# Performance work log

Measured on AMD Instinct MI355X. Metric: run time of the kernel, lower is better.

## Reference

```python
import jax, jax.numpy as jnp
import numpy as np
from jax import lax

N, L, C_IN, NOISE_C, COMP, NC = 256, 512, 514, 112, 16, 2
MAIN_IN = NOISE_C + COMP  # 128
FEAT = NC * 4 * L         # 4096

def _conv1d(x, w, b, pad):
    # x [N,C,L], w [O,I,K]
    y = lax.conv_general_dilated(x, w, (1,), [(pad, pad)], dimension_numbers=('NCH', 'OIH', 'NCH'))
    return y + b[None, :, None]

def _bn(x, g, b):
    # BatchNorm1d, training mode: biased batch stats over (N, L)
    m = x.mean(axis=(0, 2), keepdims=True)
    v = x.var(axis=(0, 2), keepdims=True)
    return (x - m) * lax.rsqrt(v + 1e-5) * g[None, :, None] + b[None, :, None]

def _lrelu(x):
    return jnp.where(x >= 0, x, 0.2 * x)

def _pos_encode(length, dim):
    j = np.arange(dim)
    div = 1.0 / np.power(10000.0, 2 * (j[:, None] // 2) / dim)   # [dim,1]
    ang = np.arange(length)[None, :] * div                       # [dim,length]
    ang = np.where((j % 2 == 0)[:, None], np.sin(ang), np.cos(ang))
    return jnp.asarray(ang[None], jnp.float32)                   # [1,dim,length]

def _assemble(circle_prob, slider_prob):
    # Vectorized run-length label expansion equivalent to the per-sample python while-loop.
    # circle_prob [N, L/2, 2], slider_prob [N, L/4, 2] -> [N, L, 3]
    n, B = slider_prob.shape[0], slider_prob.shape[1]
    c = jnp.argmax(circle_prob, -1)
    s = jnp.argmax(slider_prob, -1)
    zc = jnp.zeros(circle_prob.shape[:-1] + (1,), circle_prob.dtype)
    zs = jnp.zeros(slider_prob.shape[:-1] + (1,), slider_prob.dtype)
    cp3 = jnp.concatenate([circle_prob, zc], -1)                                   # insert 0 at class 2
    sp3 = jnp.concatenate([slider_prob[..., :1], zs, slider_prob[..., 1:]], -1)    # insert 0 at class 1
    pad100 = jnp.array([1., 0., 0.], cp3.dtype)
    pad001 = jnp.array([0., 0., 1.], cp3.dtype)
    bidx = jnp.arange(B)[None, :]
    # slider-body blocks: slider run continues and not cut by sequence end
    body = (s == 1) & (bidx < B - 1)
    prev_body = jnp.concatenate([jnp.zeros((n, 1), bool), body[:, :-1]], 1)
    # tail block ends a slider run (either run stops, or boundary block)
    tail = ((s == 1) & (bidx == B - 1)) | ((s == 0) & prev_body)
    # circle emission for each half-step: prob row if predicted circle else pad
    cr0 = jnp.where((c == 1)[..., None], cp3, pad100).reshape(n, B, 2, 3)
    bodyE = body[..., None]
    row0 = jnp.where((body | tail)[..., None], sp3, cr0[:, :, 0, :])
    row1 = jnp.where(bodyE, pad001, pad100)
    row2 = jnp.where(bodyE, pad001, cr0[:, :, 1, :])
    row3 = jnp.where(bodyE, pad001, pad100)
    return jnp.stack([row0, row1, row2, row3], 2).reshape(n, 4 * B, 3)

def _forward(noise, cond_data, gumbel_u, ext_w1, ext_b1, ext_w2, ext_b2, ext_bn_g, ext_bn_b,
             m_w1, m_b1, m_w2, m_b2, m_bn_g, m_bn_b, lin_w, lin_b, circ_w, circ_b, slid_w, slid_b):
    # FeatureExtractor
    x = cond_data.transpose(0, 2, 1)                      # [N, 514, L]
    x = _lrelu(_conv1d(x, ext_w1, ext_b1, 0))             # [N, 32, L]
    cond = _bn(_conv1d(x, ext_w2, ext_b2, 1), ext_bn_g, ext_bn_b)  # [N, 16, L]
    gen_in = jnp.concatenate([cond, noise.transpose(0, 2, 1)], 1) + _pos_encode(L, MAIN_IN)  # [N,128,L]
    h = _lrelu(_conv1d(gen_in, m_w1, m_b1, 3))            # [N, 32, L]
    h = _lrelu(_bn(_conv1d(h, m_w2, m_b2, 1), m_bn_g, m_bn_b))     # [N, 8, L]
    flat = _lrelu(h.reshape(h.shape[0], -1) @ lin_w + lin_b)       # [N, 4096]
    circle_prob = (flat @ circ_w + circ_b).reshape(-1, L // 2, NC)
    slider_prob = (flat @ slid_w + slid_b).reshape(-1, L // 4, NC)
    out = _assemble(circle_prob, slider_prob)             # [N, L, 3]
    # gumbel_softmax(hard=True, tau=1)
    g = -jnp.log(-jnp.log(gumbel_u + 1e-10) + 1e-10)
    logits = out + g
    y_soft = jax.nn.softmax(logits, -1)
    y_hard = jax.nn.one_hot(jnp.argmax(logits, -1), 3, dtype=y_soft.dtype)
    gen_out = y_hard + y_soft - lax.stop_gradient(y_soft)
    return gen_out, cond

def setup_inputs() -> dict:
    key = jax.random.key(0)
    ks = jax.random.split(key, 12)
    def rn(k, shape, fan_in):
        return jax.random.normal(k, shape, jnp.float32) * (1.0 / fan_in) ** 0.5
    return {
        'noise': jax.random.normal(ks[0], (N, L, NOISE_C), jnp.float32),
        'cond_data': jax.random.normal(ks[1], (N, L, C_IN), jnp.float32),
        'gumbel_u': jax.random.uniform(ks[2], (N, L, 3), jnp.float32),
        'ext_w1': rn(ks[3], (C_IN // 16, C_IN, 1), C_IN), 'ext_b1': jnp.zeros(C_IN // 16),
        'ext_w2': rn(ks[4], (COMP, C_IN // 16, 3), 3 * (C_IN // 16)), 'ext_b2': jnp.zeros(COMP),
        'ext_bn_g': jnp.ones(COMP), 'ext_bn_b': jnp.zeros(COMP),
        'm_w1': rn(ks[5], (NC * 16, MAIN_IN, 7), 7 * MAIN_IN), 'm_b1': jnp.zeros(NC * 16),
        'm_w2': rn(ks[6], (NC * 4, NC * 16, 3), 3 * NC * 16), 'm_b2': jnp.zeros(NC * 4),
        'm_bn_g': jnp.ones(NC * 4), 'm_bn_b': jnp.zeros(NC * 4),
        'lin_w': rn(ks[7], (FEAT, FEAT), FEAT), 'lin_b': jnp.zeros(FEAT),
        'circ_w': rn(ks[8], (FEAT, NC * L // 2), FEAT), 'circ_b': jnp.zeros(NC * L // 2),
        'slid_w': rn(ks[9], (FEAT, NC * L // 4), FEAT), 'slid_b': jnp.zeros(NC * L // 4),
    }

def reference(noise, cond_data, gumbel_u, ext_w1, ext_b1, ext_w2, ext_b2, ext_bn_g, ext_bn_b,
              m_w1, m_b1, m_w2, m_b2, m_bn_g, m_bn_b, lin_w, lin_b, circ_w, circ_b, slid_w, slid_b):
    return _forward(noise, cond_data, gumbel_u, ext_w1, ext_b1, ext_w2, ext_b2, ext_bn_g, ext_bn_b,
                    m_w1, m_b1, m_w2, m_b2, m_bn_g, m_bn_b, lin_w, lin_b, circ_w, circ_b, slid_w, slid_b)
```

## Files before the change

kernel.cpp:

```cpp
#include <hip/hip_runtime.h>
#include <math.h>

#define NB 256
#define LL 512
#define CIN 514

__device__ __forceinline__ float lrelu(float x) { return x >= 0.f ? x : 0.2f * x; }

__global__ __launch_bounds__(256) void k_pos(float* __restrict__ pos) {
    int idx = blockIdx.x * 256 + threadIdx.x;
    int c = idx >> 9, l = idx & 511;
    double e = (double)(2 * (c >> 1)) / 128.0;
    double dv = 1.0 / pow(10000.0, e);
    double a = (double)l * dv;
    pos[idx] = (float)((c & 1) ? cos(a) : sin(a));
}

__global__ __launch_bounds__(256) void k_posconv(const float* __restrict__ POS, const float* __restrict__ W,
                                                 const float* __restrict__ bias, float* __restrict__ PC) {
    const int t = threadIdx.x;
    const int o = blockIdx.x >> 4, l0 = (blockIdx.x & 15) * 32;
    const int l = l0 + (t & 31), cs = t >> 5;
    float acc = 0.f;
    for (int ci = 0; ci < 16; ++ci) {
        int c = cs * 16 + ci;
        float wv[7];
#pragma unroll
        for (int k = 0; k < 7; ++k) wv[k] = W[o * 896 + c * 7 + k];
#pragma unroll
        for (int k = 0; k < 7; ++k) {
            int gl = l + k - 3;
            if (gl >= 0 && gl < LL) acc += wv[k] * POS[c * LL + gl];
        }
    }
    __shared__ float red[8][33];
    red[cs][t & 31] = acc;
    __syncthreads();
    if (cs == 0) {
        float s = bias[o];
#pragma unroll
        for (int j = 0; j < 8; ++j) s += red[j][t & 31];
        PC[o * LL + l0 + (t & 31)] = s;
    }
}

__global__ __launch_bounds__(256) void k_conv1(const float* __restrict__ X, const float* __restrict__ W,
                                               float* __restrict__ P0, float* __restrict__ P1) {
    __shared__ __align__(16) float As[16][524];
    __shared__ __align__(16) float Bs[16][36];
    const int t = threadIdx.x;
    const int n = blockIdx.x >> 1, z = blockIdx.x & 1;
    const int kbase = z * 256;
    const int nch = z ? 17 : 16;
    const int tl = t & 63, to = t >> 6;
    const size_t rowbase = (size_t)n * 512 * CIN;

    float acc[8][8];
#pragma unroll
    for (int oi = 0; oi < 8; ++oi)
#pragma unroll
        for (int p = 0; p < 8; ++p) acc[oi][p] = 0.f;

    float2 pf[16];
    float2 pfb;

    {
        const int kb = kbase;
#pragma unroll
        for (int ps = 0; ps < 16; ++ps) {
            int idx = ps * 256 + t;
            int pos = idx >> 3, kp = idx & 7;
            int gk = kb + kp * 2;
            float2 v = {0.f, 0.f};
            if (gk + 1 < CIN) v = *(const float2*)(X + rowbase + (size_t)pos * CIN + gk);
            else if (gk < CIN) v.x = X[rowbase + (size_t)pos * CIN + gk];
            pf[ps] = v;
        }
        {
            int o = t >> 3, kp = t & 7;
            int gk = kb + kp * 2;
            float2 v = {0.f, 0.f};
            if (gk + 1 < CIN) v = *(const float2*)(W + (size_t)o * CIN + gk);
            else if (gk < CIN) v.x = W[(size_t)o * CIN + gk];
            pfb = v;
        }
#pragma unroll
        for (int ps = 0; ps < 16; ++ps) {
            int idx = ps * 256 + t;
            int pos = idx >> 3, kp = idx & 7;
            As[kp * 2][pos] = pf[ps].x;
            As[kp * 2 + 1][pos] = pf[ps].y;
        }
        {
            int o = t >> 3, kp = t & 7;
            Bs[kp * 2][o] = pfb.x;
            Bs[kp * 2 + 1][o] = pfb.y;
        }
    }
    __syncthreads();

    for (int c = 0; c < nch; ++c) {
        if (c + 1 < nch) {
            const int kb = kbase + (c + 1) * 16;
#pragma unroll
            for (int ps = 0; ps < 16; ++ps) {
                int idx = ps * 256 + t;
                int pos = idx >> 3, kp = idx & 7;
                int gk = kb + kp * 2;
                float2 v = {0.f, 0.f};
                if (gk + 1 < CIN) v = *(const float2*)(X + rowbase + (size_t)pos * CIN + gk);
                else if (gk < CIN) v.x = X[rowbase + (size_t)pos * CIN + gk];
                pf[ps] = v;
            }
            int o = t >> 3, kp = t & 7;
            int gk = kb + kp * 2;
            float2 v = {0.f, 0.f};
            if (gk + 1 < CIN) v = *(const float2*)(W + (size_t)o * CIN + gk);
            else if (gk < CIN) v.x = W[(size_t)o * CIN + gk];
            pfb = v;
        }
#pragma unroll
        for (int kk = 0; kk < 16; ++kk) {
            float4 aL = *(const float4*)&As[kk][tl * 4];
            float4 aH = *(const float4*)&As[kk][256 + tl * 4];
            float4 b0 = *(const float4*)&Bs[kk][to * 8];
            float4 b1 = *(const float4*)&Bs[kk][to * 8 + 4];
            float av[8] = {aL.x, aL.y, aL.z, aL.w, aH.x, aH.y, aH.z, aH.w};
            float bv[8] = {b0.x, b0.y, b0.z, b0.w, b1.x, b1.y, b1.z, b1.w};
#pragma unroll
            for (int oi = 0; oi < 8; ++oi)
#pragma unroll
                for (int p = 0; p < 8; ++p) acc[oi][p] += av[p] * bv[oi];
        }
        __syncthreads();
        if (c + 1 < nch) {
#pragma unroll
            for (int ps = 0; ps < 16; ++ps) {
                int idx = ps * 256 + t;
                int pos = idx >> 3, kp = idx & 7;
                As[kp * 2][pos] = pf[ps].x;
                As[kp * 2 + 1][pos] = pf[ps].y;
            }
            int o = t >> 3, kp = t & 7;
            Bs[kp * 2][o] = pfb.x;
            Bs[kp * 2 + 1][o] = pfb.y;
        }
        __syncthreads();
    }

    float* P = z ? P1 : P0;
#pragma unroll
    for (int oi = 0; oi < 8; ++oi) {
        int o = to * 8 + oi;
        float4 v0 = {acc[oi][0], acc[oi][1], acc[oi][2], acc[oi][3]};
        float4 v1 = {acc[oi][4], acc[oi][5], acc[oi][6], acc[oi][7]};
        *(float4*)(P + ((size_t)n * 32 + o) * LL + tl * 4) = v0;
        *(float4*)(P + ((size_t)n * 32 + o) * LL + 256 + tl * 4) = v1;
    }
}

__global__ __launch_bounds__(256) void k_conv2(const float* __restrict__ P0, const float* __restrict__ P1,
                                               const float* __restrict__ b1, const float* __restrict__ W,
                                               const float* __restrict__ bias, float* __restrict__ out) {
    __shared__ __align__(16) float Xs[32][264];
    __shared__ __align__(16) float Ws[16][32][4];
    const int t = threadIdx.x;
    const int n = blockIdx.x >> 1, l0 = (blockIdx.x & 1) * 256;
    for (int idx = t; idx < 32 * 258; idx += 256) {
        int i = idx / 258, j = idx % 258;
        int gl = l0 - 1 + j;
        float v = 0.f;
        if (gl >= 0 && gl < LL) {
            size_t off = ((size_t)n * 32 + i) * LL + gl;
            v = lrelu(P0[off] + P1[off] + b1[i]);
        }
        Xs[i][j] = v;
    }
    for (int idx = t; idx < 1536; idx += 256) {
        int o = idx / 96, r = idx % 96;
        Ws[o][r / 3][r % 3] = W[idx];
    }
    __syncthreads();
    const int tx = t & 31, ty = t >> 5;
    float acc[2][8];
#pragma unroll
    for (int q = 0; q < 2; ++q)
#pragma unroll
        for (int p = 0; p < 8; ++p) acc[q][p] = 0.f;
    for (int i = 0; i < 32; ++i) {
        float4 a0 = *(const float4*)&Xs[i][tx*8];
        float4 a1 = *(const float4*)&Xs[i][tx*8+4];
        float4 a2 = *(const float4*)&Xs[i][tx*8+8];
        float a[12] = {a0.x,a0.y,a0.z,a0.w,a1.x,a1.y,a1.z,a1.w,a2.x,a2.y,a2.z,a2.w};
#pragma unroll
        for (int q = 0; q < 2; ++q) {
            float4 b = *(const float4*)&Ws[ty*2+q][i][0];
#pragma unroll
            for (int p = 0; p < 8; ++p)
                acc[q][p] += a[p]*b.x + a[p+1]*b.y + a[p+2]*b.z;
        }
    }
#pragma unroll
    for (int q = 0; q < 2; ++q) {
        int o = ty*2+q; float bb = bias[o];
#pragma unroll
        for (int h = 0; h < 2; ++h) {
            float4 v;
            v.x = acc[q][h*4+0] + bb; v.y = acc[q][h*4+1] + bb;
            v.z = acc[q][h*4+2] + bb; v.w = acc[q][h*4+3] + bb;
            *(float4*)(out + ((size_t)n*16 + o)*LL + l0 + tx*8 + h*4) = v;
        }
    }
}

__global__ __launch_bounds__(256) void k_redstats(const float* __restrict__ src, int C, float* __restrict__ part) {
    const int ch = blockIdx.x, sl = blockIdx.y, t = threadIdx.x;
    float s = 0.f, q = 0.f;
    for (int i = t; i < 4096; i += 256) {
        int n = sl*8 + (i >> 9), l = i & 511;
        float v = src[((size_t)n*C + ch)*LL + l];
        s += v; q += v*v;
    }
    __shared__ float rs[256], rq[256];
    rs[t] = s; rq[t] = q;
    __syncthreads();
    for (int off = 128; off > 0; off >>= 1) {
        if (t < off) { rs[t] += rs[t+off]; rq[t] += rq[t+off]; }
        __syncthreads();
    }
    if (t == 0) { part[(ch*32+sl)*2] = rs[0]; part[(ch*32+sl)*2+1] = rq[0]; }
}

__global__ void k_bnfinal(const float* __restrict__ part, const float* __restrict__ g,
                          const float* __restrict__ b, int C, float* __restrict__ ss) {
    int ch = threadIdx.x;
    if (ch >= C) return;
    float s = 0.f, q = 0.f;
    for (int j = 0; j < 32; ++j) { s += part[(ch*32 + j)*2]; q += part[(ch*32 + j)*2 + 1]; }
    float mean = s * (1.f/131072.f);
    float var = q * (1.f/131072.f) - mean*mean;
    float sc = g[ch] / sqrtf(var + 1e-5f);
    ss[ch] = sc;
    ss[C + ch] = b[ch] - mean * sc;
}

__global__ __launch_bounds__(256) void k_bnapply(const float* __restrict__ src, const float* __restrict__ ss,
        int C, float* __restrict__ dst, int act, int total4) {
    int i4 = blockIdx.x * 256 + threadIdx.x;
    if (i4 >= total4) return;
    int i = i4 << 2;
    int ch = (i >> 9) % C;
    float sc = ss[ch], sh = ss[C + ch];
    float4 v = reinterpret_cast<const float4*>(src)[i4];
    v.x = v.x*sc + sh; v.y = v.y*sc + sh; v.z = v.z*sc + sh; v.w = v.w*sc + sh;
    if (act) { v.x = lrelu(v.x); v.y = lrelu(v.y); v.z = lrelu(v.z); v.w = lrelu(v.w); }
    reinterpret_cast<float4*>(dst)[i4] = v;
}

__global__ __launch_bounds__(256) void k_mconv1(const float* __restrict__ C16, const float* __restrict__ NZ,
        const float* __restrict__ PC, const float* __restrict__ W,
        float* __restrict__ out0, float* __restrict__ out1) {
    __shared__ __align__(16) float Gs[16][264];
    __shared__ __align__(16) float Ws[32][16][8];
    const int t = threadIdx.x;
    const int n = blockIdx.x >> 2, l0 = ((blockIdx.x >> 1) & 1) * 256, z = blockIdx.x & 1;
    const int tx = t & 31, ty = t >> 5;
    float acc[4][8];
#pragma unroll
    for (int q = 0; q < 4; ++q)
#pragma unroll
        for (int p = 0; p < 8; ++p) acc[q][p] = 0.f;

    for (int cc = 0; cc < 4; ++cc) {
        const int ctg = z * 4 + cc;
        if (cc) __syncthreads();
        if (ctg == 0) {
            for (int idx = t; idx < 16*262; idx += 256) {
                int c = idx / 262, j = idx - c * 262;
                int gl = l0 - 3 + j;
                float v = 0.f;
                if (gl >= 0 && gl < LL) v = C16[((size_t)n*16 + c)*LL + gl];
                Gs[c][j] = v;
            }
        } else {
            int nc0 = ctg * 16 - 16;
            for (int idx = t; idx < 16*262; idx += 256) {
                int c = idx & 15, j = idx >> 4;
                int gl = l0 - 3 + j;
                float v = 0.f;
                if (gl >= 0 && gl < LL) v = NZ[((size_t)n*LL + gl)*112 + nc0 + c];
                Gs[c][j] = v;
            }
        }
        for (int idx = t; idx < 32*112; idx += 256) {
            int o = idx / 112, r = idx % 112;
            Ws[o][r / 7][r % 7] = W[(size_t)o*896 + ctg*112 + r];
        }
        __syncthreads();
        for (int ci = 0; ci < 16; ++ci) {
            float4 a0 = *(const float4*)&Gs[ci][tx*4];
            float4 a1 = *(const float4*)&Gs[ci][tx*4+4];
            float4 a2 = *(const float4*)&Gs[ci][tx*4+8];
            float4 a3 = *(const float4*)&Gs[ci][128+tx*4];
            float4 a4 = *(const float4*)&Gs[ci][128+tx*4+4];
            float4 a5 = *(const float4*)&Gs[ci][128+tx*4+8];
            float aA[12] = {a0.x,a0.y,a0.z,a0.w,a1.x,a1.y,a1.z,a1.w,a2.x,a2.y,a2.z,a2.w};
            float aB[12] = {a3.x,a3.y,a3.z,a3.w,a4.x,a4.y,a4.z,a4.w,a5.x,a5.y,a5.z,a5.w};
#pragma unroll
            for (int q = 0; q < 4; ++q) {
                float4 b0 = *(const float4*)&Ws[ty*4+q][ci][0];
                float4 b1 = *(const float4*)&Ws[ty*4+q][ci][4];
                float b[7] = {b0.x,b0.y,b0.z,b0.w,b1.x,b1.y,b1.z};
#pragma unroll
                for (int p = 0; p < 4; ++p) {
#pragma unroll
                    for (int k = 0; k < 7; ++k) {
                        acc[q][p]   += aA[p+k]*b[k];
                        acc[q][4+p] += aB[p+k]*b[k];
                    }
                }
            }
        }
    }
    float* out = z ? out1 : out0;
#pragma unroll
    for (int q = 0; q < 4; ++q) {
        int o = ty*4 + q;
        float4 p0 = {0.f,0.f,0.f,0.f}, p1 = {0.f,0.f,0.f,0.f};
        if (z == 0) {
            p0 = *(const float4*)(PC + o*LL + l0 + tx*4);
            p1 = *(const float4*)(PC + o*LL + l0 + 128 + tx*4);
        }
        float4 v0 = {acc[q][0]+p0.x, acc[q][1]+p0.y, acc[q][2]+p0.z, acc[q][3]+p0.w};
        float4 v1 = {acc[q][4]+p1.x, acc[q][5]+p1.y, acc[q][6]+p1.z, acc[q][7]+p1.w};
        *(float4*)(out + ((size_t)n*32 + o)*LL + l0 + tx*4) = v0;
        *(float4*)(out + ((size_t)n*32 + o)*LL + l0 + 128 + tx*4) = v1;
    }
}

__global__ __launch_bounds__(256) void k_mconv2(const float* __restrict__ P0, const float* __restrict__ P1,
        const float* __restrict__ W, const float* __restrict__ bias, float* __restrict__ out) {
    __shared__ __align__(16) float Xs[32][264];
    __shared__ __align__(16) float Ws[8][32][4];
    const int t = threadIdx.x;
    const int n = blockIdx.x >> 1, l0 = (blockIdx.x & 1) * 256;
    for (int idx = t; idx < 32 * 258; idx += 256) {
        int i = idx / 258, j = idx % 258;
        int gl = l0 - 1 + j;
        float v = 0.f;
        if (gl >= 0 && gl < LL) {
            size_t off = ((size_t)n * 32 + i) * LL + gl;
            v = lrelu(P0[off] + P1[off]);
        }
        Xs[i][j] = v;
    }
    for (int idx = t; idx < 768; idx += 256) {
        int o = idx / 96, r = idx % 96;
        Ws[o][r / 3][r % 3] = W[idx];
    }
    __syncthreads();
    const int tx = t & 31, ty = t >> 5;
    float acc[8];
#pragma unroll
    for (int p = 0; p < 8; ++p) acc[p] = 0.f;
    for (int i = 0; i < 32; ++i) {
        float4 a0 = *(const float4*)&Xs[i][tx*8];
        float4 a1 = *(const float4*)&Xs[i][tx*8+4];
        float4 a2 = *(const float4*)&Xs[i][tx*8+8];
        float a[12] = {a0.x,a0.y,a0.z,a0.w,a1.x,a1.y,a1.z,a1.w,a2.x,a2.y,a2.z,a2.w};
        float4 b = *(const float4*)&Ws[ty][i][0];
#pragma unroll
        for (int p = 0; p < 8; ++p)
            acc[p] += a[p]*b.x + a[p+1]*b.y + a[p+2]*b.z;
    }
    float bb = bias[ty];
#pragma unroll
    for (int h = 0; h < 2; ++h) {
        float4 v;
        v.x = acc[h*4+0] + bb; v.y = acc[h*4+1] + bb;
        v.z = acc[h*4+2] + bb; v.w = acc[h*4+3] + bb;
        *(float4*)(out + ((size_t)n*8 + ty)*LL + l0 + tx*8 + h*4) = v;
    }
}

__global__ __launch_bounds__(256) void k_lin(const float* __restrict__ A, const float* __restrict__ B,
                                             float* __restrict__ part) {
    __shared__ __align__(16) float As[32][68];
    __shared__ __align__(16) float Bs[32][68];
    const int t = threadIdx.x;
    const int bid = blockIdx.x;
    const int xcd = bid & 7, idx = bid >> 3;
    const int f0 = (xcd * 8 + (idx >> 4)) * 64;
    const int sub = idx & 15;
    const int m0 = (sub & 3) * 64;
    const int z = sub >> 2;
    const int lane = t & 63, wv = t >> 6;
    const int smi = t & 63, skq = t >> 6;
    const int ski = t >> 3, sf4 = t & 7;
    const int k0base = z * 1024;

    const int ar = wv * 16 + ((lane >> 4) << 2);
    const int br = (lane & 15) << 2;

    float acc[4][4];
#pragma unroll
    for (int i = 0; i < 4; ++i)
#pragma unroll
        for (int q = 0; q < 4; ++q) acc[i][q] = 0.f;

    for (int it = 0; it < 32; ++it) {
        const int k0 = k0base + it * 32;
        {
            const float* pA = A + (size_t)(m0 + smi) * 4096 + k0;
            float4 a0 = *(const float4*)(pA + skq * 4);
            float4 a1 = *(const float4*)(pA + skq * 4 + 16);
            const float* pB = B + (size_t)(k0 + ski) * 4096 + f0;
            float4 b0 = *(const float4*)(pB + sf4 * 4);
            float4 b1 = *(const float4*)(pB + sf4 * 4 + 32);
            As[skq*4+0][smi] = a0.x; As[skq*4+1][smi] = a0.y; As[skq*4+2][smi] = a0.z; As[skq*4+3][smi] = a0.w;
            As[skq*4+16][smi] = a1.x; As[skq*4+17][smi] = a1.y; As[skq*4+18][smi] = a1.z; As[skq*4+19][smi] = a1.w;
            *(float4*)&Bs[ski][sf4*4] = b0;
            *(float4*)&Bs[ski][sf4*4+32] = b1;
        }
        __syncthreads();
#pragma unroll
        for (int kk = 0; kk < 32; ++kk) {
            float4 a = *(const float4*)&As[kk][ar];
            float4 b = *(const float4*)&Bs[kk][br];
            float av[4] = {a.x, a.y, a.z, a.w};
            float bv[4] = {b.x, b.y, b.z, b.w};
#pragma unroll
            for (int i = 0; i < 4; ++i)
#pragma unroll
                for (int q = 0; q < 4; ++q) acc[i][q] += av[i] * bv[q];
        }
        __syncthreads();
    }

#pragma unroll
    for (int i = 0; i < 4; ++i) {
        int m = m0 + ar + i;
        float4 v = {acc[i][0], acc[i][1], acc[i][2], acc[i][3]};
        *(float4*)(part + ((size_t)z * 256 + m) * 4096 + f0 + br) = v;
    }
}

__global__ __launch_bounds__(256) void k_linred(const float* __restrict__ part, const float* __restrict__ bias,
        float* __restrict__ out) {
    int i4 = blockIdx.x*256 + threadIdx.x;
    int i = i4 << 2;
    int f = i & 4095;
    float4 a = ((const float4*)part)[i4];
    float4 b = ((const float4*)(part + 1048576))[i4];
    float4 c = ((const float4*)(part + 2097152))[i4];
    float4 d = ((const float4*)(part + 3145728))[i4];
    float4 bb = *(const float4*)(bias + f);
    float4 r;
    r.x = lrelu(a.x + b.x + c.x + d.x + bb.x);
    r.y = lrelu(a.y + b.y + c.y + d.y + bb.y);
    r.z = lrelu(a.z + b.z + c.z + d.z + bb.z);
    r.w = lrelu(a.w + b.w + c.w + d.w + bb.w);
    ((float4*)out)[i4] = r;
}

__global__ __launch_bounds__(256) void k_heads(const float* __restrict__ A, const float* __restrict__ CW,
        const float* __restrict__ SW, float* __restrict__ part) {
    __shared__ __align__(16) float As[32][36];
    __shared__ __align__(16) float Bs[32][132];
    const int t = threadIdx.x;
    const int m0 = blockIdx.x * 32, f0 = blockIdx.y * 128, z = blockIdx.z;
    const float* B; int ldb, fb;
    if (f0 < 512) { B = CW; ldb = 512; fb = f0; } else { B = SW; ldb = 256; fb = f0 - 512; }
    const int tm = t & 7, tf = t >> 3;
    const int mi = t >> 3, kq = t & 7;
    float acc[4][4];
#pragma unroll
    for (int pm = 0; pm < 4; ++pm)
#pragma unroll
        for (int pf = 0; pf < 4; ++pf) acc[pm][pf] = 0.f;
    for (int k0 = z * 512; k0 < z * 512 + 512; k0 += 32) {
        float4 av = *(const float4*)(A + (size_t)(m0 + mi) * 4096 + k0 + kq * 4);
        As[kq*4+0][mi] = av.x; As[kq*4+1][mi] = av.y; As[kq*4+2][mi] = av.z; As[kq*4+3][mi] = av.w;
#pragma unroll
        for (int pass = 0; pass < 4; ++pass) {
            int fi = pass * 32 + kq * 4;
            *(float4*)&Bs[mi][fi] = *(const float4*)(B + (size_t)(k0 + mi) * ldb + fb + fi);
        }
        __syncthreads();
#pragma unroll 8
        for (int kk = 0; kk < 32; ++kk) {
            float4 a = *(const float4*)&As[kk][tm * 4];
            float4 b = *(const float4*)&Bs[kk][tf * 4];
            float avv[4] = {a.x,a.y,a.z,a.w};
            float bvv[4] = {b.x,b.y,b.z,b.w};
#pragma unroll
            for (int pm = 0; pm < 4; ++pm)
#pragma unroll
                for (int pf = 0; pf < 4; ++pf) acc[pm][pf] += avv[pm]*bvv[pf];
        }
        __syncthreads();
    }
#pragma unroll
    for (int pm = 0; pm < 4; ++pm) {
        float4 v = {acc[pm][0], acc[pm][1], acc[pm][2], acc[pm][3]};
        *(float4*)(part + ((size_t)z * 256 + m0 + tm * 4 + pm) * 768 + f0 + tf * 4) = v;
    }
}

__global__ __launch_bounds__(256) void k_headred(const float* __restrict__ part, const float* __restrict__ cb,
        const float* __restrict__ sb, float* __restrict__ circ, float* __restrict__ slid) {
    int i4 = blockIdx.x * 256 + threadIdx.x;
    int i = i4 << 2;
    int n = i / 768, f = i % 768;
    float4 s = {0.f,0.f,0.f,0.f};
#pragma unroll
    for (int ks = 0; ks < 8; ++ks) {
        float4 p = *(const float4*)(part + ((size_t)ks*256 + n)*768 + f);
        s.x += p.x; s.y += p.y; s.z += p.z; s.w += p.w;
    }
    if (f < 512) {
        float4 bb = *(const float4*)(cb + f);
        s.x += bb.x; s.y += bb.y; s.z += bb.z; s.w += bb.w;
        *(float4*)(circ + (size_t)n*512 + f) = s;
    } else {
        float4 bb = *(const float4*)(sb + f - 512);
        s.x += bb.x; s.y += bb.y; s.z += bb.z; s.w += bb.w;
        *(float4*)(slid + (size_t)n*256 + f - 512) = s;
    }
}

__global__ __launch_bounds__(128) void k_assemble(const float* __restrict__ circ, const float* __restrict__ slid,
        const float* __restrict__ gum, float* __restrict__ out) {
    const int n = blockIdx.x;
    const int b = threadIdx.x;
    const float* sp = slid + (size_t)n * 256;
    const float* cp = circ + (size_t)n * 512;
    float sl0 = sp[2*b], sl1 = sp[2*b+1];
    int s = sl1 > sl0 ? 1 : 0;
    int prevb = 0;
    if (b > 0) prevb = (sp[2*b-1] > sp[2*b-2]) ? 1 : 0;
    bool body = (s == 1) && (b < 127);
    bool tail = ((s == 1) && (b == 127)) || ((s == 0) && (prevb == 1));
    float c0a = cp[4*b], c0b = cp[4*b+1], c1a = cp[4*b+2], c1b = cp[4*b+3];
    bool cA = c0b > c0a, cB = c1b > c1a;
    float rows[4][3];
    if (body || tail)      { rows[0][0]=sl0; rows[0][1]=0.f; rows[0][2]=sl1; }
    else if (cA)           { rows[0][0]=c0a; rows[0][1]=c0b; rows[0][2]=0.f; }
    else                   { rows[0][0]=1.f; rows[0][1]=0.f; rows[0][2]=0.f; }
    if (body)              { rows[1][0]=0.f; rows[1][1]=0.f; rows[1][2]=1.f; }
    else                   { rows[1][0]=1.f; rows[1][1]=0.f; rows[1][2]=0.f; }
    if (body)              { rows[2][0]=0.f; rows[2][1]=0.f; rows[2][2]=1.f; }
    else if (cB)           { rows[2][0]=c1a; rows[2][1]=c1b; rows[2][2]=0.f; }
    else                   { rows[2][0]=1.f; rows[2][1]=0.f; rows[2][2]=0.f; }
    rows[3][0]=rows[1][0]; rows[3][1]=rows[1][1]; rows[3][2]=rows[1][2];
#pragma unroll
    for (int r = 0; r < 4; ++r) {
        int l = 4*b + r;
        const float* u = gum + ((size_t)n*512 + l)*3;
        float g0 = -logf(-logf(u[0]+1e-10f)+1e-10f);
        float g1 = -logf(-logf(u[1]+1e-10f)+1e-10f);
        float g2 = -logf(-logf(u[2]+1e-10f)+1e-10f);
        float t0 = rows[r][0]+g0, t1 = rows[r][1]+g1, t2 = rows[r][2]+g2;
        int am = 0; float mv = t0;
        if (t1 > mv) { am = 1; mv = t1; }
        if (t2 > mv) { am = 2; mv = t2; }
        float e0 = expf(t0-mv), e1 = expf(t1-mv), e2 = expf(t2-mv);
        float ssum = e0+e1+e2;
        float y0 = e0/ssum, y1 = e1/ssum, y2 = e2/ssum;
        float* o = out + ((size_t)n*512 + l)*3;
        o[0] = ((am==0?1.f:0.f) + y0) - y0;
        o[1] = ((am==1?1.f:0.f) + y1) - y1;
        o[2] = ((am==2?1.f:0.f) + y2) - y2;
    }
}

extern "C" void kernel_launch(void* const* d_in, const int* in_sizes, int n_in,
                              void* d_out, int out_size, void* d_ws, size_t ws_size,
                              hipStream_t stream) {
    const float* noise   = (const float*)d_in[0];
    const float* cond    = (const float*)d_in[1];
    const float* gumbel  = (const float*)d_in[2];
    const float* ext_w1  = (const float*)d_in[3];
    const float* ext_b1  = (const float*)d_in[4];
    const float* ext_w2  = (const float*)d_in[5];
    const float* ext_b2  = (const float*)d_in[6];
    const float* ext_bng = (const float*)d_in[7];
    const float* ext_bnb = (const float*)d_in[8];
    const float* m_w1    = (const float*)d_in[9];
    const float* m_b1    = (const float*)d_in[10];
    const float* m_w2    = (const float*)d_in[11];
    const float* m_b2    = (const float*)d_in[12];
    const float* m_bng   = (const float*)d_in[13];
    const float* m_bnb   = (const float*)d_in[14];
    const float* lin_w   = (const float*)d_in[15];
    const float* lin_b   = (const float*)d_in[16];
    const float* circ_w  = (const float*)d_in[17];
    const float* circ_b  = (const float*)d_in[18];
    const float* slid_w  = (const float*)d_in[19];
    const float* slid_b  = (const float*)d_in[20];

    float* genout  = (float*)d_out;
    float* condout = (float*)d_out + 256*512*3;

    float* w     = (float*)d_ws;
    float* x1    = w;
    float* y2    = x1 + 4194304;
    float* posb  = y2 + 2097152;
    float* circ  = posb + 65536;
    float* slid  = circ + 131072;
    float* flatB = slid + 65536;
    float* partL = flatB + 1048576;
    float* partH = partL + 2097152;
    float* stats = partH + 1572864;
    float* pc    = stats + 4096;
    float* buf1  = flatB;

    k_pos<<<256, 256, 0, stream>>>(posb);
    k_posconv<<<512, 256, 0, stream>>>(posb, m_w1, m_b1, pc);
    k_conv1<<<512, 256, 0, stream>>>(cond, ext_w1, x1, buf1);
    k_conv2<<<512, 256, 0, stream>>>(x1, buf1, ext_b1, ext_w2, ext_b2, y2);
    k_redstats<<<dim3(16,32), 256, 0, stream>>>(y2, 16, stats);
    k_bnfinal<<<1, 64, 0, stream>>>(stats, ext_bng, ext_bnb, 16, stats + 2048);
    k_bnapply<<<2048, 256, 0, stream>>>(y2, stats + 2048, 16, condout, 0, 524288);
    k_mconv1<<<1024, 256, 0, stream>>>(condout, noise, pc, m_w1, x1, buf1);
    k_mconv2<<<512, 256, 0, stream>>>(x1, buf1, m_w2, m_b2, y2);
    k_redstats<<<dim3(8,32), 256, 0, stream>>>(y2, 8, stats);
    k_bnfinal<<<1, 64, 0, stream>>>(stats, m_bng, m_bnb, 8, stats + 2048 + 64);
    k_bnapply<<<1024, 256, 0, stream>>>(y2, stats + 2048 + 64, 8, y2, 1, 262144);
    k_lin<<<1024, 256, 0, stream>>>(y2, lin_w, x1);
    k_linred<<<1024, 256, 0, stream>>>(x1, lin_b, flatB);
    k_heads<<<dim3(8,6,8), 256, 0, stream>>>(flatB, circ_w, slid_w, partH);
    k_headred<<<192, 256, 0, stream>>>(partH, circ_b, slid_b, circ, slid);
    k_assemble<<<256, 128, 0, stream>>>(circ, slid, gumbel, genout);
}
```

Baseline: 554.7 us.

## Register-prefetch next channel group in mconv1 to overlap loads with compute

The mconv1 kernel now loads the next channel group's input slice and weights into registers while computing on the current group in shared memory, then stores them to shared memory between two barriers. This software pipelining is meant to hide global-memory latency that previously stalled each of the four channel-group iterations. The shared tile row stride also changes from 264 to 268, which alters bank mapping for the transposed stores. The prefetch costs 31 extra registers per thread and may reduce occupancy.

```diff
diff --git a/kernel.cpp b/kernel.cpp
--- a/kernel.cpp
+++ b/kernel.cpp
@@ -260,7 +260,7 @@
 __global__ __launch_bounds__(256) void k_mconv1(const float* __restrict__ C16, const float* __restrict__ NZ,
         const float* __restrict__ PC, const float* __restrict__ W,
         float* __restrict__ out0, float* __restrict__ out1) {
-    __shared__ __align__(16) float Gs[16][264];
+    __shared__ __align__(16) float Gs[16][268];
     __shared__ __align__(16) float Ws[32][16][8];
     const int t = threadIdx.x;
     const int n = blockIdx.x >> 2, l0 = ((blockIdx.x >> 1) & 1) * 256, z = blockIdx.x & 1;
@@ -271,32 +271,77 @@
 #pragma unroll
         for (int p = 0; p < 8; ++p) acc[q][p] = 0.f;
 
-    for (int cc = 0; cc < 4; ++cc) {
-        const int ctg = z * 4 + cc;
-        if (cc) __syncthreads();
-        if (ctg == 0) {
-            for (int idx = t; idx < 16*262; idx += 256) {
-                int c = idx / 262, j = idx - c * 262;
-                int gl = l0 - 3 + j;
-                float v = 0.f;
-                if (gl >= 0 && gl < LL) v = C16[((size_t)n*16 + c)*LL + gl];
-                Gs[c][j] = v;
-            }
-        } else {
-            int nc0 = ctg * 16 - 16;
-            for (int idx = t; idx < 16*262; idx += 256) {
+    float gpf[17];
+    float wpf[14];
+
+    if (z == 0) {
+        for (int idx = t; idx < 16*262; idx += 256) {
+            int c = idx / 262, j = idx - c*262;
+            int gl = l0 - 3 + j;
+            float v = 0.f;
+            if (gl >= 0 && gl < LL) v = C16[((size_t)n*16 + c)*LL + gl];
+            Gs[c][j] = v;
+        }
+#pragma unroll
+        for (int p = 0; p < 14; ++p) {
+            int idx = p * 256 + t;
+            int o = idx / 112, r = idx - o * 112;
+            Ws[o][r / 7][r % 7] = W[(size_t)o*896 + r];
+        }
+    } else {
+#pragma unroll
+        for (int p = 0; p < 17; ++p) {
+            int idx = p * 256 + t;
+            float v = 0.f;
+            if (idx < 4192) {
                 int c = idx & 15, j = idx >> 4;
                 int gl = l0 - 3 + j;
+                if (gl >= 0 && gl < LL) v = NZ[((size_t)n*LL + gl)*112 + 48 + c];
+            }
+            gpf[p] = v;
+        }
+#pragma unroll
+        for (int p = 0; p < 14; ++p) {
+            int idx = p * 256 + t;
+            int o = idx / 112, r = idx - o * 112;
+            wpf[p] = W[(size_t)o*896 + 4*112 + r];
+        }
+#pragma unroll
+        for (int p = 0; p < 17; ++p) {
+            int idx = p * 256 + t;
+            if (idx < 4192) Gs[idx & 15][idx >> 4] = gpf[p];
+        }
+#pragma unroll
+        for (int p = 0; p < 14; ++p) {
+            int idx = p * 256 + t;
+            int o = idx / 112, r = idx - o * 112;
+            Ws[o][r / 7][r % 7] = wpf[p];
+        }
+    }
+    __syncthreads();
+
+    for (int cc = 0; cc < 4; ++cc) {
+        if (cc < 3) {
+            const int nctg = z * 4 + cc + 1;
+            const int nc0 = nctg * 16 - 16;
+#pragma unroll
+            for (int p = 0; p < 17; ++p) {
+                int idx = p * 256 + t;
                 float v = 0.f;
-                if (gl >= 0 && gl < LL) v = NZ[((size_t)n*LL + gl)*112 + nc0 + c];
-                Gs[c][j] = v;
-            }
-        }
-        for (int idx = t; idx < 32*112; idx += 256) {
-            int o = idx / 112, r = idx % 112;
-            Ws[o][r / 7][r % 7] = W[(size_t)o*896 + ctg*112 + r];
-        }
-        __syncthreads();
+                if (idx < 4192) {
+                    int c = idx & 15, j = idx >> 4;
+                    int gl = l0 - 3 + j;
+                    if (gl >= 0 && gl < LL) v = NZ[((size_t)n*LL + gl)*112 + nc0 + c];
+                }
+                gpf[p] = v;
+            }
+#pragma unroll
+            for (int p = 0; p < 14; ++p) {
+                int idx = p * 256 + t;
+                int o = idx / 112, r = idx - o * 112;
+                wpf[p] = W[(size_t)o*896 + nctg*112 + r];
+            }
+        }
         for (int ci = 0; ci < 16; ++ci) {
             float4 a0 = *(const float4*)&Gs[ci][tx*4];
             float4 a1 = *(const float4*)&Gs[ci][tx*4+4];
@@ -321,7 +366,23 @@
                 }
             }
         }
-    }
+        if (cc < 3) {
+            __syncthreads();
+#pragma unroll
+            for (int p = 0; p < 17; ++p) {
+                int idx = p * 256 + t;
+                if (idx < 4192) Gs[idx & 15][idx >> 4] = gpf[p];
+            }
+#pragma unroll
+            for (int p = 0; p < 14; ++p) {
+                int idx = p * 256 + t;
+                int o = idx / 112, r = idx - o * 112;
+                Ws[o][r / 7][r % 7] = wpf[p];
+            }
+            __syncthreads();
+        }
+    }
+
     float* out = z ? out1 : out0;
 #pragma unroll
     for (int q = 0; q < 4; ++q) {
```

Result: faster. 538.0 us (-3.0%).
